# Kernel optimization log

Hardware: AMD Instinct MI355X
Metric: run time of the kernel (lower is better)

## Reference

```python
import jax, jax.numpy as jnp
import numpy as np

D_MODEL = 1024
NUM_HEADS = 16
HEAD_DIM = D_MODEL // NUM_HEADS
B, S = 2, 2048


def setup_inputs() -> dict:
    key = jax.random.key(0)
    ks = jax.random.split(key, 8)
    scale = 1.0 / np.sqrt(D_MODEL)
    inp = {
        "query": jax.random.normal(ks[0], (B, S, D_MODEL), jnp.float32),
        "key": jax.random.normal(ks[1], (B, S, D_MODEL), jnp.float32),
        "value": jax.random.normal(ks[2], (B, S, D_MODEL), jnp.float32),
        # causal mask, broadcastable over batch and heads
        "mask": jnp.tril(jnp.ones((S, S), dtype=bool))[None, None, :, :],
        # torch nn.Linear weights: y = x @ W.T (+ b)
        "Wq": jax.random.normal(ks[3], (D_MODEL, D_MODEL), jnp.float32) * scale,
        "Wk": jax.random.normal(ks[4], (D_MODEL, D_MODEL), jnp.float32) * scale,
        "Wv": jax.random.normal(ks[5], (D_MODEL, D_MODEL), jnp.float32) * scale,
        "Wo": jax.random.normal(ks[6], (D_MODEL, D_MODEL), jnp.float32) * scale,
        "bo": jax.random.normal(ks[7], (D_MODEL,), jnp.float32) * scale,
    }
    return inp


def _split_heads(x):
    b, s, _ = x.shape
    return x.reshape(b, s, NUM_HEADS, HEAD_DIM).transpose(0, 2, 1, 3)  # [B,H,S,Dh]


def reference(query, key, value, mask, Wq, Wk, Wv, Wo, bo):
    q = _split_heads(query @ Wq.T)
    k = _split_heads(key @ Wk.T)
    v = _split_heads(value @ Wv.T)
    scores = jnp.einsum("bhqd,bhkd->bhqk", q, k) / jnp.sqrt(jnp.float32(HEAD_DIM))
    scores = jnp.where(mask, scores, jnp.float32(-jnp.inf))
    attn = jax.nn.softmax(scores, axis=-1)
    out = jnp.einsum("bhqk,bhkd->bhqd", attn, v)  # [B,H,S,Dh]
    out = out.transpose(0, 2, 1, 3).reshape(query.shape[0], q.shape[2], D_MODEL)
    return out @ Wo.T + bo
```

## Files before the change

### kernel.cpp

```cpp
#include <hip/hip_runtime.h>
#include <hip/hip_bf16.h>

#define DM   1024
#define NH   16
#define HD   64
#define SEQ  2048
#define BATCH 2
#define MTOT (BATCH*SEQ)

typedef unsigned short u16;
typedef __attribute__((ext_vector_type(8))) short bf16x8;
typedef __attribute__((ext_vector_type(4))) float f32x4;

#define SC2F 0.1803368801111464f

__device__ __forceinline__ float bf2f(u16 h) {
  union { unsigned int i; float f; } u; u.i = ((unsigned int)h) << 16; return u.f;
}
__device__ __forceinline__ u16 f2bf(float f) {
  union { float f; unsigned int i; } u; u.f = f;
  unsigned int r = u.i + 0x7fffu + ((u.i >> 16) & 1u);
  return (u16)(r >> 16);
}
__device__ __forceinline__ unsigned int pk2(float lo, float hi) {
  union { float f; unsigned int u; } a, b; a.f = lo; b.f = hi;
  return ((a.u + 0x8000u) >> 16) | ((b.u + 0x8000u) & 0xFFFF0000u);
}
__device__ __forceinline__ unsigned int cvtpk(float lo, float hi) {
  unsigned int r;
  asm("v_cvt_pk_bf16_f32 %0, %1, %2" : "=v"(r) : "v"(lo), "v"(hi));
  return r;
}

__device__ __forceinline__ uint4 load8_bf16(const void* base, size_t elemOff, bool isf32) {
  if (!isf32) return *(const uint4*)((const u16*)base + elemOff);
  const float* f = (const float*)base + elemOff;
  f32x4 a = *(const f32x4*)f;
  f32x4 b = *(const f32x4*)(f + 4);
  union { u16 h[8]; uint4 v; } r;
  r.h[0]=f2bf(a[0]); r.h[1]=f2bf(a[1]); r.h[2]=f2bf(a[2]); r.h[3]=f2bf(a[3]);
  r.h[4]=f2bf(b[0]); r.h[5]=f2bf(b[1]); r.h[6]=f2bf(b[2]); r.h[7]=f2bf(b[3]);
  return r.v;
}

__global__ __launch_bounds__(256) void prep(
    const void* __restrict__ q, const void* __restrict__ k, const void* __restrict__ v,
    const void* __restrict__ wq, const void* __restrict__ wk, const void* __restrict__ wv,
    const void* __restrict__ wo, const void* __restrict__ bo,
    u16* __restrict__ Xq, u16* __restrict__ Xk, u16* __restrict__ Xv,
    u16* __restrict__ Wqb, u16* __restrict__ Wkb, u16* __restrict__ Wvb, u16* __restrict__ Wob,
    float* __restrict__ biasf, int* __restrict__ flag_out)
{
  const int tid = threadIdx.x;
  __shared__ int cnts[4];
  {
    const u16* qs = (const u16*)q;
    int e0 = (qs[tid*2]   >> 7) & 0xFF;
    int e1 = (qs[tid*2+1] >> 7) & 0xFF;
    int c = ((e0 >= 0x6E && e0 <= 0x8F) ? 1 : 0) + ((e1 >= 0x6E && e1 <= 0x8F) ? 1 : 0);
    c += __shfl_xor(c, 1);  c += __shfl_xor(c, 2);  c += __shfl_xor(c, 4);
    c += __shfl_xor(c, 8);  c += __shfl_xor(c, 16); c += __shfl_xor(c, 32);
    if ((tid & 63) == 0) cnts[tid >> 6] = c;
  }
  __syncthreads();
  const bool isf32 = (cnts[0] + cnts[1] + cnts[2] + cnts[3]) < 400;

  const int z = blockIdx.z;
  if (z == 7) {
    if (blockIdx.x == 0) {
      if (tid == 0) *flag_out = isf32 ? 0 : 1;
      for (int i = tid; i < DM; i += 256)
        biasf[i] = isf32 ? ((const float*)bo)[i] : bf2f(((const u16*)bo)[i]);
    }
    return;
  }
  const void* src; u16* dst; size_t n;
  switch (z) {
    case 0: src=q;  dst=Xq;  n=(size_t)MTOT*DM; break;
    case 1: src=k;  dst=Xk;  n=(size_t)MTOT*DM; break;
    case 2: src=v;  dst=Xv;  n=(size_t)MTOT*DM; break;
    case 3: src=wq; dst=Wqb; n=(size_t)DM*DM;   break;
    case 4: src=wk; dst=Wkb; n=(size_t)DM*DM;   break;
    case 5: src=wv; dst=Wvb; n=(size_t)DM*DM;   break;
    default: src=wo; dst=Wob; n=(size_t)DM*DM;  break;
  }
  const size_t stride = (size_t)gridDim.x * 256 * 8;
  for (size_t i = ((size_t)blockIdx.x * 256 + tid) * 8; i < n; i += stride)
    *(uint4*)(dst + i) = load8_bf16(src, i, isf32);
}

__device__ __forceinline__ void gld16(const u16* g, u16* l) {
  __builtin_amdgcn_global_load_lds(
      (const __attribute__((address_space(1))) void*)g,
      (__attribute__((address_space(3))) void*)l, 16, 0, 0);
}

__global__ __launch_bounds__(256) void gemm_qkv(
    const u16* __restrict__ X0, const u16* __restrict__ X1, const u16* __restrict__ X2,
    const u16* __restrict__ W0, const u16* __restrict__ W1, const u16* __restrict__ W2,
    u16* __restrict__ F0, u16* __restrict__ F1, u16* __restrict__ F2)
{
  __shared__ __align__(16) u16 smem[16384];
  u16* const A0 = smem;
  u16* const A1 = smem + 4096;
  u16* const B0 = smem + 8192;
  u16* const B1 = smem + 12288;

  const int zz = blockIdx.z;
  const u16* X = (zz==0) ? X0 : ((zz==1) ? X1 : X2);
  const u16* W = (zz==0) ? W0 : ((zz==1) ? W1 : W2);
  u16* outF    = (zz==0) ? F0 : ((zz==1) ? F1 : F2);

  const int tid = threadIdx.x;
  const int wave = tid >> 6, lane = tid & 63, quad = lane >> 4, l16 = lane & 15;
  const int wr = wave >> 1, wc = wave & 1;
  const int m0 = blockIdx.x * 128, n0 = blockIdx.y * 128;

  const int sg = ((lane & 3) ^ ((lane >> 3) & 3)) * 8;
  const int rS = wave*32 + (lane >> 2);
  const u16* gA0 = X + (size_t)(m0 + rS)*DM + sg;
  const u16* gA1 = X + (size_t)(m0 + rS + 16)*DM + sg;
  const u16* gB0 = W + (size_t)(n0 + rS)*DM + sg;
  const u16* gB1 = W + (size_t)(n0 + rS + 16)*DM + sg;
  const int so = wave*1024;

  const int xslot8 = (quad ^ ((l16 >> 1) & 3)) * 8;

  f32x4 acc[4][4];
#pragma unroll
  for (int i = 0; i < 4; i++)
#pragma unroll
    for (int j = 0; j < 4; j++) { acc[i][j][0]=0.f; acc[i][j][1]=0.f; acc[i][j][2]=0.f; acc[i][j][3]=0.f; }

  gld16(gA0, A0 + so);
  gld16(gA1, A0 + so + 512);
  gld16(gB0, B0 + so);
  gld16(gB1, B0 + so + 512);
  asm volatile("" ::: "memory");

  for (int k0 = 0; k0 < DM; k0 += 32) {
    const int cb = (k0 >> 5) & 1;
    u16* const Ab = cb ? A1 : A0;
    u16* const Bb = cb ? B1 : B0;
    if (k0 + 32 < DM) {
      u16* const An = cb ? A0 : A1;
      u16* const Bn = cb ? B0 : B1;
      gld16(gA0 + k0 + 32, An + so);
      gld16(gA1 + k0 + 32, An + so + 512);
      gld16(gB0 + k0 + 32, Bn + so);
      gld16(gB1 + k0 + 32, Bn + so + 512);
      asm volatile("s_waitcnt vmcnt(4)" ::: "memory");
    } else {
      asm volatile("s_waitcnt vmcnt(0)" ::: "memory");
    }
    __builtin_amdgcn_s_barrier();
    asm volatile("" ::: "memory");

    bf16x8 af[4], bfr[4];
#pragma unroll
    for (int fr = 0; fr < 4; fr++)
      af[fr] = *(const bf16x8*)&Ab[(wr*64 + fr*16 + l16)*32 + xslot8];
#pragma unroll
    for (int fc = 0; fc < 4; fc++)
      bfr[fc] = *(const bf16x8*)&Bb[(wc*64 + fc*16 + l16)*32 + xslot8];
#pragma unroll
    for (int fr = 0; fr < 4; fr++)
#pragma unroll
      for (int fc = 0; fc < 4; fc++)
        acc[fr][fc] = __builtin_amdgcn_mfma_f32_16x16x32_bf16(af[fr], bfr[fc], acc[fr][fc], 0, 0, 0);

    asm volatile("" ::: "memory");
    __builtin_amdgcn_s_barrier();
    asm volatile("" ::: "memory");
  }

  if (zz == 2) {
    u16* const Ts = smem;
    const int bb = m0 >> 11;
    const int s0 = m0 & (SEQ-1);
#pragma unroll
    for (int p = 0; p < 2; p++) {
      __syncthreads();
      if (wc == p) {
#pragma unroll
        for (int fr = 0; fr < 4; fr++) {
#pragma unroll
          for (int fc = 0; fc < 4; fc++) {
            const int dl = fc*16 + l16;
            const int sb = wr*64 + fr*16 + quad*4;
            const int slot = (sb >> 3) ^ (dl & 15);
            u16* rowp = &Ts[dl*128 + slot*8 + (sb & 7)];
            *(unsigned int*)(rowp)     = pk2(acc[fr][fc][0], acc[fr][fc][1]);
            *(unsigned int*)(rowp + 2) = pk2(acc[fr][fc][2], acc[fr][fc][3]);
          }
        }
      }
      __syncthreads();
      const int dl2 = tid >> 2, ch4 = tid & 3;
      const int hh = (n0 + p*64) >> 6;
      u16* dst = outF + ((size_t)(bb*NH + hh)*HD + dl2)*SEQ + s0 + ch4*32;
#pragma unroll
      for (int j = 0; j < 4; j++) {
        const int c  = ch4*4 + j;
        const int lo = (c >> 2)*32 + (c & 3)*4;
        const int hi = lo + 16;
        uint2 lo2 = *(const uint2*)&Ts[dl2*128 + (((lo >> 3) ^ (dl2 & 15))*8) + (lo & 7)];
        uint2 hi2 = *(const uint2*)&Ts[dl2*128 + (((hi >> 3) ^ (dl2 & 15))*8) + (hi & 7)];
        uint4 o; o.x = lo2.x; o.y = lo2.y; o.z = hi2.x; o.w = hi2.y;
        *(uint4*)&dst[j*8] = o;
      }
    }
    return;
  }

#pragma unroll
  for (int fr = 0; fr < 4; fr++) {
#pragma unroll
    for (int rr = 0; rr < 4; rr++) {
      const int m = m0 + wr*64 + fr*16 + quad*4 + rr;
#pragma unroll
      for (int fc = 0; fc < 4; fc++) {
        const int n = n0 + wc*64 + fc*16 + l16;
        float vv = acc[fr][fc][rr];
        if (zz == 0) vv *= SC2F;
        const int b = m >> 11, s = m & (SEQ-1), h = n >> 6, d = n & (HD-1);
        outF[((size_t)(b*NH + h)*SEQ + s)*HD + d] = f2bf(vv);
      }
    }
  }
}

__global__ __launch_bounds__(256) void gemm_out(
    const u16* __restrict__ X, const u16* __restrict__ W,
    const float* __restrict__ biasf, void* __restrict__ outP,
    const int* __restrict__ dflag)
{
  __shared__ __align__(16) u16 smem[12288];
  u16* const A0 = smem;
  u16* const A1 = smem + 4096;
  u16* const B0 = smem + 8192;
  u16* const B1 = smem + 10240;

  const int tid = threadIdx.x;
  const int wave = tid >> 6, lane = tid & 63, quad = lane >> 4, l16 = lane & 15;
  const int wr = wave >> 1, wc = wave & 1;
  const int m0 = blockIdx.x * 128, n0 = blockIdx.y * 64;

  const int sg = ((lane & 3) ^ ((lane >> 3) & 3)) * 8;
  const int rA = wave*32 + (lane >> 2);
  const int rB = wave*16 + (lane >> 2);
  const u16* gA0 = X + (size_t)(m0 + rA)*DM + sg;
  const u16* gA1 = X + (size_t)(m0 + rA + 16)*DM + sg;
  const u16* gB0 = W + (size_t)(n0 + rB)*DM + sg;
  const int soA = wave*1024, soB = wave*512;

  const int xslot8 = (quad ^ ((l16 >> 1) & 3)) * 8;

  f32x4 acc[4][2];
#pragma unroll
  for (int i = 0; i < 4; i++)
#pragma unroll
    for (int j = 0; j < 2; j++) { acc[i][j][0]=0.f; acc[i][j][1]=0.f; acc[i][j][2]=0.f; acc[i][j][3]=0.f; }

  gld16(gA0, A0 + soA);
  gld16(gA1, A0 + soA + 512);
  gld16(gB0, B0 + soB);
  asm volatile("" ::: "memory");

  for (int k0 = 0; k0 < DM; k0 += 32) {
    const int cb = (k0 >> 5) & 1;
    u16* const Ab = cb ? A1 : A0;
    u16* const Bb = cb ? B1 : B0;
    if (k0 + 32 < DM) {
      u16* const An = cb ? A0 : A1;
      u16* const Bn = cb ? B0 : B1;
      gld16(gA0 + k0 + 32, An + soA);
      gld16(gA1 + k0 + 32, An + soA + 512);
      gld16(gB0 + k0 + 32, Bn + soB);
      asm volatile("s_waitcnt vmcnt(3)" ::: "memory");
    } else {
      asm volatile("s_waitcnt vmcnt(0)" ::: "memory");
    }
    __builtin_amdgcn_s_barrier();
    asm volatile("" ::: "memory");

    bf16x8 af[4], bfr[2];
#pragma unroll
    for (int fr = 0; fr < 4; fr++)
      af[fr] = *(const bf16x8*)&Ab[(wr*64 + fr*16 + l16)*32 + xslot8];
#pragma unroll
    for (int fc = 0; fc < 2; fc++)
      bfr[fc] = *(const bf16x8*)&Bb[(wc*32 + fc*16 + l16)*32 + xslot8];
#pragma unroll
    for (int fr = 0; fr < 4; fr++)
#pragma unroll
      for (int fc = 0; fc < 2; fc++)
        acc[fr][fc] = __builtin_amdgcn_mfma_f32_16x16x32_bf16(af[fr], bfr[fc], acc[fr][fc], 0, 0, 0);

    asm volatile("" ::: "memory");
    __builtin_amdgcn_s_barrier();
    asm volatile("" ::: "memory");
  }

  const bool isf32 = (*dflag == 0);
#pragma unroll
  for (int fr = 0; fr < 4; fr++) {
#pragma unroll
    for (int rr = 0; rr < 4; rr++) {
      const int m = m0 + wr*64 + fr*16 + quad*4 + rr;
#pragma unroll
      for (int fc = 0; fc < 2; fc++) {
        const int n = n0 + wc*32 + fc*16 + l16;
        float vv = acc[fr][fc][rr] + biasf[n];
        if (isf32) ((float*)outP)[(size_t)m*DM + n] = vv;
        else       ((u16*)outP)[(size_t)m*DM + n]   = f2bf(vv);
      }
    }
  }
}

__global__ __launch_bounds__(256) void attn_mfma(
    const u16* __restrict__ Qb, const u16* __restrict__ Kb,
    const u16* __restrict__ Vtb,
    u16* __restrict__ Opart, float* __restrict__ mlpart)
{
  __shared__ u16 Ks[2][64*64];
  __shared__ u16 Vs[2][64*64];

  const int bh = blockIdx.x;
  const int pr = blockIdx.y, z = blockIdx.z;
  const u16* Qp = Qb  + (size_t)bh * SEQ * HD;
  const u16* Kp = Kb  + (size_t)bh * SEQ * HD;
  const u16* Vp = Vtb + (size_t)bh * HD * SEQ;

  const int tid  = threadIdx.x;
  const int wave = tid >> 6, lane = tid & 63, quad = lane >> 4, l16 = lane & 15;

  const int i0 = wave*128 + lane, i1 = i0 + 64;
  const int r0 = i0 >> 3, c0 = (i0 & 7) ^ (r0 & 7);
  const int r1 = i1 >> 3, c1 = (i1 & 7) ^ (r1 & 7);
  const int kq_off0 = r0*HD + c0*8;
  const int kq_off1 = r1*HD + c1*8;
  const int v_off0  = r0*SEQ + c0*8;
  const int v_off1  = r1*SEQ + c1*8;

  const int l7 = l16 & 7;
  const int ql = wave*16 + l16;
  const int so = wave*1024;

  for (int ph = 0; ph < 2; ph++) {
    const int qt = ph ? (31 - pr) : pr;
    const int n = qt + 1, half = (n + 1) >> 1;
    const int klo = z ? half : 0, khi = z ? n : half;
    const int q0 = qt * 64;
    const int qg = q0 + ql;

    const u16* qrow = Qp + (size_t)qg * HD;
    const bf16x8 bq0 = *(const bf16x8*)(qrow + quad*8);
    const bf16x8 bq1 = *(const bf16x8*)(qrow + 32 + quad*8);

    f32x4 O[4];
#pragma unroll
    for (int u = 0; u < 4; u++) { O[u][0]=0.f; O[u][1]=0.f; O[u][2]=0.f; O[u][3]=0.f; }
    float mi = -__builtin_inff();
    f32x4 lv = {0.f, 0.f, 0.f, 0.f};

    if (klo < khi) {
      gld16(Kp + klo*(64*HD) + kq_off0, &Ks[0][so]);
      gld16(Kp + klo*(64*HD) + kq_off1, &Ks[0][so + 512]);
      gld16(Vp + klo*64 + v_off0, &Vs[0][so]);
      gld16(Vp + klo*64 + v_off1, &Vs[0][so + 512]);
    }
    asm volatile("" ::: "memory");

    for (int kt = klo; kt < khi; kt++) {
      const int cb = (kt - klo) & 1;
      const u16* kb = &Ks[cb][0];
      const u16* vb = &Vs[cb][0];
      if (kt + 1 < khi) {
        u16* kn = &Ks[cb ^ 1][so];
        u16* vn = &Vs[cb ^ 1][so];
        gld16(Kp + (kt+1)*(64*HD) + kq_off0, kn);
        gld16(Kp + (kt+1)*(64*HD) + kq_off1, kn + 512);
        gld16(Vp + (kt+1)*64 + v_off0, vn);
        gld16(Vp + (kt+1)*64 + v_off1, vn + 512);
        asm volatile("s_waitcnt vmcnt(4)" ::: "memory");
      } else {
        asm volatile("s_waitcnt vmcnt(0)" ::: "memory");
      }
      __builtin_amdgcn_s_barrier();
      asm volatile("" ::: "memory");

      f32x4 st[4];
#pragma unroll
      for (int t = 0; t < 4; t++) { st[t][0]=0.f; st[t][1]=0.f; st[t][2]=0.f; st[t][3]=0.f; }
#pragma unroll
      for (int s = 0; s < 2; s++) {
        const bf16x8 bq = s ? bq1 : bq0;
        const int ch = s*4 + quad;
#pragma unroll
        for (int t = 0; t < 4; t++) {
          bf16x8 ak = *(const bf16x8*)&kb[((t*16 + l16)*8 + (ch ^ l7))*8];
          st[t] = __builtin_amdgcn_mfma_f32_16x16x32_bf16(ak, bq, st[t], 0, 0, 0);
        }
      }

      if (kt == qt) {
#pragma unroll
        for (int t = 0; t < 4; t++)
#pragma unroll
          for (int r = 0; r < 4; r++)
            if (kt*64 + t*16 + quad*4 + r > qg) st[t][r] = -__builtin_inff();
      }

      f32x4 m01 = __builtin_elementwise_max(st[0], st[1]);
      f32x4 m23 = __builtin_elementwise_max(st[2], st[3]);
      f32x4 mm  = __builtin_elementwise_max(m01, m23);
      float mx = fmaxf(fmaxf(mm[0], mm[1]), fmaxf(mm[2], mm[3]));
      mx = fmaxf(mx, __shfl_xor(mx, 16));
      mx = fmaxf(mx, __shfl_xor(mx, 32));

      if (__any(mx > mi + 8.0f)) {
        const float nm = fmaxf(mi, mx);
        const float al = exp2f(mi - nm);
        mi = nm;
        const f32x4 alv = {al, al, al, al};
        lv *= alv;
        O[0] *= alv; O[1] *= alv; O[2] *= alv; O[3] *= alv;
      }

      const f32x4 miv = {mi, mi, mi, mi};
      unsigned int w[4][2];
      f32x4 e0, e1, e2, e3;
      {
        f32x4 d0 = st[0] - miv, d1 = st[1] - miv, d2 = st[2] - miv, d3 = st[3] - miv;
        e0[0]=exp2f(d0[0]); e0[1]=exp2f(d0[1]); e0[2]=exp2f(d0[2]); e0[3]=exp2f(d0[3]);
        e1[0]=exp2f(d1[0]); e1[1]=exp2f(d1[1]); e1[2]=exp2f(d1[2]); e1[3]=exp2f(d1[3]);
        e2[0]=exp2f(d2[0]); e2[1]=exp2f(d2[1]); e2[2]=exp2f(d2[2]); e2[3]=exp2f(d2[3]);
        e3[0]=exp2f(d3[0]); e3[1]=exp2f(d3[1]); e3[2]=exp2f(d3[2]); e3[3]=exp2f(d3[3]);
      }
      w[0][0] = cvtpk(e0[0], e0[1]); w[0][1] = cvtpk(e0[2], e0[3]);
      w[1][0] = cvtpk(e1[0], e1[1]); w[1][1] = cvtpk(e1[2], e1[3]);
      w[2][0] = cvtpk(e2[0], e2[1]); w[2][1] = cvtpk(e2[2], e2[3]);
      w[3][0] = cvtpk(e3[0], e3[1]); w[3][1] = cvtpk(e3[2], e3[3]);
      lv += (e0 + e1) + (e2 + e3);

#pragma unroll
      for (int s = 0; s < 2; s++) {
        union { unsigned int u[4]; bf16x8 v; } bp;
        bp.u[0] = w[2*s][0];   bp.u[1] = w[2*s][1];
        bp.u[2] = w[2*s+1][0]; bp.u[3] = w[2*s+1][1];
        const int ch = s*4 + quad;
#pragma unroll
        for (int u = 0; u < 4; u++) {
          bf16x8 av = *(const bf16x8*)&vb[((u*16 + l16)*8 + (ch ^ l7))*8];
          O[u] = __builtin_amdgcn_mfma_f32_16x16x32_bf16(av, bp.v, O[u], 0, 0, 0);
        }
      }

      asm volatile("" ::: "memory");
      __builtin_amdgcn_s_barrier();
      asm volatile("" ::: "memory");
    }

    float ls = (lv[0] + lv[1]) + (lv[2] + lv[3]);
    ls += __shfl_xor(ls, 16);
    ls += __shfl_xor(ls, 32);

    const int pi = (bh*32 + qt)*2 + z;
    u16* op = Opart + (size_t)pi*4096 + ql*64;
#pragma unroll
    for (int u = 0; u < 4; u++) {
      uint2 u2; u2.x = pk2(O[u][0], O[u][1]); u2.y = pk2(O[u][2], O[u][3]);
      *(uint2*)&op[u*16 + quad*4] = u2;
    }
    if (quad == 0) {
      float2 ml2; ml2.x = mi; ml2.y = ls;
      *(float2*)&mlpart[(size_t)pi*128 + ql*2] = ml2;
    }
  }
}

__global__ __launch_bounds__(64) void attn_merge(
    const u16* __restrict__ Opart, const float* __restrict__ mlpart,
    u16* __restrict__ aO)
{
  const int g = blockIdx.x;
  const int bh = g & 31, qt = g >> 5;
  const int b = bh >> 4, h = bh & 15;
  const int t = threadIdx.x;
  const int pi0 = (bh*32 + qt)*2, pi1 = pi0 + 1;

  const float2 ml0 = *(const float2*)&mlpart[(size_t)pi0*128 + t*2];
  const float2 ml1 = *(const float2*)&mlpart[(size_t)pi1*128 + t*2];
  const float M = fmaxf(ml0.x, ml1.x);
  float w0 = exp2f(ml0.x - M), w1 = exp2f(ml1.x - M);
  const float inv = 1.0f / (w0*ml0.y + w1*ml1.y);
  w0 *= inv; w1 *= inv;

  const u16* o0 = Opart + (size_t)pi0*4096 + t*64;
  const u16* o1 = Opart + (size_t)pi1*4096 + t*64;
  u16* out = aO + (size_t)(b*SEQ + qt*64 + t)*DM + h*HD;
#pragma unroll
  for (int d0 = 0; d0 < 64; d0 += 8) {
    union { uint4 v; u16 h[8]; } a, c; union { uint4 v; u16 h[8]; } bb;
    a.v  = *(const uint4*)&o0[d0];
    bb.v = *(const uint4*)&o1[d0];
#pragma unroll
    for (int j = 0; j < 8; j += 2) {
      float x0 = w0*bf2f(a.h[j])   + w1*bf2f(bb.h[j]);
      float x1 = w0*bf2f(a.h[j+1]) + w1*bf2f(bb.h[j+1]);
      unsigned int pk = pk2(x0, x1);
      c.h[j] = (u16)(pk & 0xFFFF); c.h[j+1] = (u16)(pk >> 16);
    }
    *(uint4*)&out[d0] = c.v;
  }
}

extern "C" void kernel_launch(void* const* d_in, const int* in_sizes, int n_in,
                              void* d_out, int out_size, void* d_ws, size_t ws_size,
                              hipStream_t stream) {
  const void* q  = d_in[0];
  const void* k  = d_in[1];
  const void* v  = d_in[2];
  const void* wq = d_in[4];
  const void* wk = d_in[5];
  const void* wv = d_in[6];
  const void* wo = d_in[7];
  const void* bo = d_in[8];

  const size_t TX = (size_t)MTOT*DM;
  const size_t TW = (size_t)DM*DM;
  u16* ws  = (u16*)d_ws;
  u16* Xq  = ws;
  u16* Xk  = ws + TX;
  u16* Xv  = ws + 2*TX;
  u16* Wqb = ws + 3*TX;
  u16* Wkb = Wqb + TW;
  u16* Wvb = Wqb + 2*TW;
  u16* Wob = Wqb + 3*TW;
  u16* Qw  = ws + 3*TX + 4*TW;
  u16* Kw  = Qw + TX;
  u16* Vt  = Qw + 2*TX;
  u16*   Opart  = Xk;
  float* mlpart = (float*)Wqb;
  u16*   aO     = Xq;
  float* biasf  = (float*)(Qw + 3*TX);
  int*   fl     = (int*)(biasf + DM);

  dim3 blk(256);
  prep<<<dim3(512, 1, 8), blk, 0, stream>>>(q, k, v, wq, wk, wv, wo, bo,
      Xq, Xk, Xv, Wqb, Wkb, Wvb, Wob, biasf, fl);
  gemm_qkv<<<dim3(MTOT/128, DM/128, 3), blk, 0, stream>>>(
      Xq, Xk, Xv, Wqb, Wkb, Wvb, Qw, Kw, Vt);
  attn_mfma<<<dim3(BATCH*NH, 16, 2), blk, 0, stream>>>(Qw, Kw, Vt, Opart, mlpart);
  attn_merge<<<dim3(32*32), dim3(64), 0, stream>>>(Opart, mlpart, aO);
  gemm_out<<<dim3(MTOT/128, DM/64), blk, 0, stream>>>(aO, Wob, biasf, d_out, fl);
}
```

Before: 231.1 us.

## Load K/V MFMA fragments directly from global memory instead of LDS staging

Removes the double-buffered LDS staging of K and V tiles, along with the async global-to-LDS loads, waitcnt and block barriers. Each wave now reads its MFMA operand fragments for K and V straight from global memory (via cache) every tile. This drops the barriers and LDS traffic, but every wave redundantly fetches the same K/V tiles and loses the prefetch overlap, so load latency is exposed on each iteration.

After: 310.4 us. 34.3% more time.

```diff
diff --git a/kernel.cpp b/kernel.cpp
--- a/kernel.cpp
+++ b/kernel.cpp
@@ -324,9 +324,6 @@
     const u16* __restrict__ Vtb,
     u16* __restrict__ Opart, float* __restrict__ mlpart)
 {
-  __shared__ u16 Ks[2][64*64];
-  __shared__ u16 Vs[2][64*64];
-
   const int bh = blockIdx.x;
   const int pr = blockIdx.y, z = blockIdx.z;
   const u16* Qp = Qb  + (size_t)bh * SEQ * HD;
@@ -335,25 +332,16 @@
 
   const int tid  = threadIdx.x;
   const int wave = tid >> 6, lane = tid & 63, quad = lane >> 4, l16 = lane & 15;
-
-  const int i0 = wave*128 + lane, i1 = i0 + 64;
-  const int r0 = i0 >> 3, c0 = (i0 & 7) ^ (r0 & 7);
-  const int r1 = i1 >> 3, c1 = (i1 & 7) ^ (r1 & 7);
-  const int kq_off0 = r0*HD + c0*8;
-  const int kq_off1 = r1*HD + c1*8;
-  const int v_off0  = r0*SEQ + c0*8;
-  const int v_off1  = r1*SEQ + c1*8;
-
-  const int l7 = l16 & 7;
   const int ql = wave*16 + l16;
-  const int so = wave*1024;
+
+  const u16* kfb = Kp + (size_t)l16*HD + quad*8;
+  const u16* vfb = Vp + (size_t)l16*SEQ + quad*8;
 
   for (int ph = 0; ph < 2; ph++) {
     const int qt = ph ? (31 - pr) : pr;
     const int n = qt + 1, half = (n + 1) >> 1;
     const int klo = z ? half : 0, khi = z ? n : half;
-    const int q0 = qt * 64;
-    const int qg = q0 + ql;
+    const int qg = qt*64 + ql;
 
     const u16* qrow = Qp + (size_t)qg * HD;
     const bf16x8 bq0 = *(const bf16x8*)(qrow + quad*8);
@@ -365,31 +353,16 @@
     float mi = -__builtin_inff();
     f32x4 lv = {0.f, 0.f, 0.f, 0.f};
 
-    if (klo < khi) {
-      gld16(Kp + klo*(64*HD) + kq_off0, &Ks[0][so]);
-      gld16(Kp + klo*(64*HD) + kq_off1, &Ks[0][so + 512]);
-      gld16(Vp + klo*64 + v_off0, &Vs[0][so]);
-      gld16(Vp + klo*64 + v_off1, &Vs[0][so + 512]);
-    }
-    asm volatile("" ::: "memory");
-
     for (int kt = klo; kt < khi; kt++) {
-      const int cb = (kt - klo) & 1;
-      const u16* kb = &Ks[cb][0];
-      const u16* vb = &Vs[cb][0];
-      if (kt + 1 < khi) {
-        u16* kn = &Ks[cb ^ 1][so];
-        u16* vn = &Vs[cb ^ 1][so];
-        gld16(Kp + (kt+1)*(64*HD) + kq_off0, kn);
-        gld16(Kp + (kt+1)*(64*HD) + kq_off1, kn + 512);
-        gld16(Vp + (kt+1)*64 + v_off0, vn);
-        gld16(Vp + (kt+1)*64 + v_off1, vn + 512);
-        asm volatile("s_waitcnt vmcnt(4)" ::: "memory");
-      } else {
-        asm volatile("s_waitcnt vmcnt(0)" ::: "memory");
-      }
-      __builtin_amdgcn_s_barrier();
-      asm volatile("" ::: "memory");
+      const u16* kp = kfb + (size_t)kt*(64*HD);
+      const u16* vp = vfb + (size_t)kt*64;
+
+      bf16x8 ak[2][4];
+#pragma unroll
+      for (int s = 0; s < 2; s++)
+#pragma unroll
+        for (int t = 0; t < 4; t++)
+          ak[s][t] = *(const bf16x8*)(kp + t*(16*HD) + s*32);
 
       f32x4 st[4];
 #pragma unroll
@@ -397,12 +370,9 @@
 #pragma unroll
       for (int s = 0; s < 2; s++) {
         const bf16x8 bq = s ? bq1 : bq0;
-        const int ch = s*4 + quad;
-#pragma unroll
-        for (int t = 0; t < 4; t++) {
-          bf16x8 ak = *(const bf16x8*)&kb[((t*16 + l16)*8 + (ch ^ l7))*8];
-          st[t] = __builtin_amdgcn_mfma_f32_16x16x32_bf16(ak, bq, st[t], 0, 0, 0);
-        }
+#pragma unroll
+        for (int t = 0; t < 4; t++)
+          st[t] = __builtin_amdgcn_mfma_f32_16x16x32_bf16(ak[s][t], bq, st[t], 0, 0, 0);
       }
 
       if (kt == qt) {
@@ -450,17 +420,12 @@
         union { unsigned int u[4]; bf16x8 v; } bp;
         bp.u[0] = w[2*s][0];   bp.u[1] = w[2*s][1];
         bp.u[2] = w[2*s+1][0]; bp.u[3] = w[2*s+1][1];
-        const int ch = s*4 + quad;
 #pragma unroll
         for (int u = 0; u < 4; u++) {
-          bf16x8 av = *(const bf16x8*)&vb[((u*16 + l16)*8 + (ch ^ l7))*8];
+          bf16x8 av = *(const bf16x8*)(vp + u*(16*SEQ) + s*32);
           O[u] = __builtin_amdgcn_mfma_f32_16x16x32_bf16(av, bp.v, O[u], 0, 0, 0);
         }
       }
-
-      asm volatile("" ::: "memory");
-      __builtin_amdgcn_s_barrier();
-      asm volatile("" ::: "memory");
     }
 
     float ls = (lv[0] + lv[1]) + (lv[2] + lv[3]);
```
